# Kernel optimization log

Measured on AMD Instinct MI355X. Metric: run time of the kernel, lower is better.

Reference implementation:

```python
import jax, jax.numpy as jnp
import numpy as np
from jax import lax

N_HEADS = 16
EPS = 1e-6
CHUNK = 128  # chunk size for the causal kv cumsum scan


def causal_dot_product(q, k, v):
    """Equivalent to cumsum over outer-products: out[l] = q[l] . sum_{j<=l} k[j] v[j]^T.
    Chunked lax.scan avoids materializing the [B,H,L,D,M] tensor.
    q,k: [B,H,L,D], v: [B,H,L,M] -> [B,H,L,M]."""
    B, H, L, D = q.shape
    M = v.shape[-1]
    nc = L // CHUNK
    qc = q.reshape(B, H, nc, CHUNK, D).transpose(2, 0, 1, 3, 4)
    kc = k.reshape(B, H, nc, CHUNK, D).transpose(2, 0, 1, 3, 4)
    vc = v.reshape(B, H, nc, CHUNK, M).transpose(2, 0, 1, 3, 4)

    def step(kv_carry, inp):
        qb, kb, vb = inp  # [B,H,C,D], [B,H,C,D], [B,H,C,M]
        kv = jnp.einsum('bhcd,bhcm->bhcdm', kb, vb)
        kv_cum = jnp.cumsum(kv, axis=2) + kv_carry[:, :, None]
        out = jnp.einsum('bhcd,bhcdm->bhcm', qb, kv_cum)
        return kv_cum[:, :, -1], out

    init = jnp.zeros((B, H, D, M), q.dtype)
    _, outs = lax.scan(step, init, (qc, kc, vc))  # outs: [nc,B,H,C,M]
    return outs.transpose(1, 2, 0, 3, 4).reshape(B, H, L, M)


def flow_attention_causal(x, Wq, bq, Wk, bk, Wv, bv, Wo, bo):
    B, L, _ = x.shape
    d_model = Wq.shape[1]
    H = N_HEADS
    # projections -> [B,H,L,D]
    q = (x @ Wq + bq).reshape(B, L, H, -1).transpose(0, 2, 1, 3)
    k = (x @ Wk + bk).reshape(B, L, H, -1).transpose(0, 2, 1, 3)
    v = (x @ Wv + bv).reshape(B, L, H, -1).transpose(0, 2, 1, 3)
    # kernel_method = sigmoid
    q = jax.nn.sigmoid(q)
    k = jax.nn.sigmoid(k)

    sink_incoming = 1.0 / jnp.einsum('bhld,bhld->bhl', q + EPS, jnp.cumsum(k, axis=2) + EPS)
    source_outgoing = 1.0 / jnp.einsum('bhld,bhld->bhl', k + EPS, jnp.cumsum(q, axis=2) + EPS)
    normal = (jnp.arange(L, dtype=x.dtype) + 1.0)[None, None, :]  # [1,1,L]
    sink_incoming = sink_incoming * normal
    source_outgoing = source_outgoing * normal

    conserved_sink = jnp.einsum(
        'bhld,bhld->bhl', q + EPS,
        jnp.cumsum(k * source_outgoing[..., None], axis=2) + EPS) / normal
    conserved_source = jnp.einsum(
        'bhld,bhld->bhl', k + EPS,
        jnp.cumsum(q * sink_incoming[..., None], axis=2) + EPS) / normal

    sink_allocation = jax.nn.sigmoid(conserved_sink)
    cs = jnp.exp(conserved_source)
    source_competition = cs / jnp.cumsum(cs, axis=-1) * normal

    out = causal_dot_product(
        q * (sink_incoming / normal)[..., None],
        k,
        v * source_competition[..., None]) * sink_allocation[..., None]
    out = out.transpose(0, 2, 1, 3).reshape(B, L, d_model)
    return out @ Wo + bo  # dropout is identity at eval


def setup_inputs() -> dict:
    key = jax.random.key(0)
    ks = jax.random.split(key, 9)
    B, L, d_model = 4, 4096, 1024
    s = 0.02
    return {
        'x': jax.random.normal(ks[0], (B, L, d_model), dtype=jnp.float32),
        'Wq': jax.random.normal(ks[1], (d_model, d_model), dtype=jnp.float32) * s,
        'bq': jnp.zeros((d_model,), dtype=jnp.float32),
        'Wk': jax.random.normal(ks[2], (d_model, d_model), dtype=jnp.float32) * s,
        'bk': jnp.zeros((d_model,), dtype=jnp.float32),
        'Wv': jax.random.normal(ks[3], (d_model, d_model), dtype=jnp.float32) * s,
        'bv': jnp.zeros((d_model,), dtype=jnp.float32),
        'Wo': jax.random.normal(ks[4], (d_model, d_model), dtype=jnp.float32) * s,
        'bo': jnp.zeros((d_model,), dtype=jnp.float32),
    }


def reference(x, Wq, bq, Wk, bk, Wv, bv, Wo, bo):
    return flow_attention_causal(x, Wq, bq, Wk, bk, Wv, bv, Wo, bo)
```

## Files before the change

kernel.cpp:

```cpp
#include <hip/hip_runtime.h>
#include <stdint.h>

#define B_ 4
#define L_ 4096
#define DM 1024
#define H_ 16
#define D_ 64
#define BH (B_*H_)
#define N_ (B_*L_)
#define CS 128
#define NC (L_/CS)
#define SC 64
#define NSC (L_/SC)
#define EPSF 1e-6f

typedef unsigned short u16;
typedef unsigned int   u32;
typedef __attribute__((ext_vector_type(8))) short s16x8;
typedef __attribute__((ext_vector_type(4))) float f32x4;

__device__ __forceinline__ float bf2f(u16 u){
  union { u32 i; float f; } v; v.i = ((u32)u) << 16; return v.f;
}
__device__ __forceinline__ u16 f2bf(float f){
  union { float f; u32 i; } v; v.f = f;
  u32 i = v.i;
  return (u16)((i + 0x7fffu + ((i >> 16) & 1u)) >> 16);
}
__device__ __forceinline__ void gload16(const void* g, void* l){
  __builtin_amdgcn_global_load_lds(
      (const __attribute__((address_space(1))) u32*)g,
      (__attribute__((address_space(3))) u32*)l, 16, 0, 0);
}
__device__ __forceinline__ f32x4 mfma16(s16x8 a, s16x8 b, f32x4 c){
  return __builtin_amdgcn_mfma_f32_16x16x32_bf16(a, b, c, 0, 0, 0);
}
__device__ __forceinline__ float sigmoidf_(float x){ return 1.0f/(1.0f+__expf(-x)); }

__device__ __forceinline__ float prefix_sum64(const float* __restrict__ sums,
                                              int bh, int sc, int lane){
  float run = 0.f;
  for (int g = 0; g < NSC; g += 16){
    float tv[16];
    #pragma unroll
    for (int j = 0; j < 16; j++)
      tv[j] = sums[((size_t)bh*NSC + g + j)*64 + lane];
    #pragma unroll
    for (int j = 0; j < 16; j++)
      if (g + j < sc) run += tv[j];
  }
  return run;
}

__global__ __launch_bounds__(256) void prep_kernel(
    const float* __restrict__ x,
    const float* __restrict__ Wq, const float* __restrict__ Wk,
    const float* __restrict__ Wv, const float* __restrict__ Wo,
    u16* __restrict__ xb, u16* __restrict__ wqkvT, u16* __restrict__ woT){
  __shared__ float t[64][65];
  int bid = blockIdx.x;
  if (bid < 16384){
    int i = bid * 256 + threadIdx.x;
    float4 v = ((const float4*)x)[i];
    union { u16 s[4]; uint2 u; } o;
    o.s[0]=f2bf(v.x); o.s[1]=f2bf(v.y); o.s[2]=f2bf(v.z); o.s[3]=f2bf(v.w);
    ((uint2*)xb)[i] = o.u;
    return;
  }
  int w = bid - 16384;
  int z = w >> 8, w2 = w & 255;
  const float* W = (z==0) ? Wq : (z==1) ? Wk : (z==2) ? Wv : Wo;
  u16* WT = (z<3) ? (wqkvT + (size_t)z*DM*DM) : woT;
  int n0 = (w2 & 15) * 64, k0 = (w2 >> 4) * 64;
  int tx = threadIdx.x & 63, ty = threadIdx.x >> 6;
  #pragma unroll
  for (int s = 0; s < 64; s += 4)
    t[ty + s][tx] = W[(size_t)(k0 + ty + s) * DM + n0 + tx];
  __syncthreads();
  #pragma unroll
  for (int s = 0; s < 64; s += 4)
    WT[(size_t)(n0 + ty + s) * DM + k0 + tx] = f2bf(t[tx][ty + s]);
}

template<int QKV>
__global__ __launch_bounds__(512, 2) void gemm256_kernel(
    const u16* __restrict__ A, const u16* __restrict__ BT,
    const float* __restrict__ biasq, const float* __restrict__ biask, const float* __restrict__ biasv,
    u16* __restrict__ oq, u16* __restrict__ ok, u16* __restrict__ ov,
    float* __restrict__ outf,
    float* __restrict__ sumQ, float* __restrict__ sumK, int NBY)
{
  __shared__ __align__(16) u16 smem[65536];
  char* smb = (char*)smem;
  int tid = threadIdx.x;
  int wave = tid >> 6, lane = tid & 63;
  int wm = wave >> 2, wn = wave & 3;
  int nwg = gridDim.x;
  int q8 = nwg >> 3;
  int id = blockIdx.x;
  int id2 = (id & 7) * q8 + (id >> 3);
  int bx = id2 / NBY, by = id2 % NBY;
  int m0 = bx * 256, n0 = by * 256;
  int srcq = (tid & 7) ^ ((tid >> 3) & 7);
  const u16* aRow = A  + (size_t)(m0 + (tid >> 3)) * 1024 + srcq * 8;
  const u16* bRow = BT + (size_t)(n0 + (tid >> 3)) * 1024 + srcq * 8;

  f32x4 acc[8][4];
  #pragma unroll
  for (int i=0;i<8;i++)
    #pragma unroll
    for (int j=0;j<4;j++) acc[i][j] = (f32x4){0.f,0.f,0.f,0.f};

  int fr = lane & 15, q = lane >> 4;
  int aoff0 = fr*128 + (((q ^ (lane&3)) + 4*((lane>>2)&1)) << 4);
  int aoff1 = fr*128 + (((q ^ (lane&3)) + 4*(1 ^ ((lane>>2)&1))) << 4);

  #define STAGE(s, t) { \
    _Pragma("unroll") \
    for (int i_ = 0; i_ < 4; i_++){ \
      gload16(aRow + (size_t)(t)*64 + (size_t)i_*65536, smb + (s)*32768 + i_*8192 + tid*16); \
      gload16(bRow + (size_t)(t)*64 + (size_t)i_*65536, smb + 65536 + (s)*32768 + i_*8192 + tid*16); \
    } }

  #define COMPUTE(s) { \
    const char* Ab_ = smb + (s)*32768 + wm*16384; \
    const char* Bb_ = smb + 65536 + (s)*32768 + wn*8192; \
    _Pragma("unroll") \
    for (int kk_ = 0; kk_ < 2; kk_++){ \
      int off_ = kk_ ? aoff1 : aoff0; \
      s16x8 af_[8], bf_[4]; \
      _Pragma("unroll") \
      for (int mi_ = 0; mi_ < 8; mi_++) af_[mi_] = *(const s16x8*)(Ab_ + mi_*2048 + off_); \
      _Pragma("unroll") \
      for (int ni_ = 0; ni_ < 4; ni_++) bf_[ni_] = *(const s16x8*)(Bb_ + ni_*2048 + off_); \
      _Pragma("unroll") \
      for (int mi_ = 0; mi_ < 8; mi_++) \
        _Pragma("unroll") \
        for (int ni_ = 0; ni_ < 4; ni_++) \
          acc[mi_][ni_] = mfma16(af_[mi_], bf_[ni_], acc[mi_][ni_]); \
    } }

  STAGE(0, 0)
  STAGE(1, 1)
  for (int t = 0; t < 14; t++){
    asm volatile("s_waitcnt vmcnt(8)" ::: "memory");
    __builtin_amdgcn_s_barrier();
    asm volatile("" ::: "memory");
    COMPUTE(t & 1)
    asm volatile("s_waitcnt lgkmcnt(0)" ::: "memory");
    __builtin_amdgcn_s_barrier();
    asm volatile("" ::: "memory");
    STAGE(t & 1, t + 2)
  }
  asm volatile("s_waitcnt vmcnt(8)" ::: "memory");
  __builtin_amdgcn_s_barrier();
  asm volatile("" ::: "memory");
  COMPUTE(0)
  asm volatile("s_waitcnt vmcnt(0)" ::: "memory");
  __builtin_amdgcn_s_barrier();
  asm volatile("" ::: "memory");
  COMPUTE(1)

  int colblk = n0 + wn*64;
  int which  = QKV ? (colblk >> 10) : 0;
  int cl0    = QKV ? (colblk & 1023) : colblk;
  const float* bias = QKV ? (which==0 ? biasq : (which==1 ? biask : biasv)) : biasq;
  u16* outp = QKV ? (which==0 ? oq : (which==1 ? ok : ov)) : (u16*)0;
  float cs0[4] = {0.f,0.f,0.f,0.f}, cs1[4] = {0.f,0.f,0.f,0.f};
  #pragma unroll
  for (int mi = 0; mi < 8; mi++){
    int row = m0 + wm*128 + mi*16 + (lane>>4)*4;
    #pragma unroll
    for (int ni = 0; ni < 4; ni++){
      int cl = cl0 + ni*16 + fr;
      float bv = bias[cl];
      #pragma unroll
      for (int r = 0; r < 4; r++){
        float val = acc[mi][ni][r] + bv;
        if (QKV){
          if (which < 2) val = sigmoidf_(val);
          outp[(size_t)(row + r) * 1024 + cl] = f2bf(val);
          if (which < 2){ if (mi < 4) cs0[ni] += val; else cs1[ni] += val; }
        } else {
          outf[(size_t)(row + r) * 1024 + cl] = val;
        }
      }
    }
  }
  if (QKV && which < 2){
    float* sums = (which==0) ? sumQ : sumK;
    int bh = (m0 >> 12) * H_ + ((colblk & 1023) >> 6);
    int sc0 = ((m0 & 4095) >> 6) + wm*2;
    #pragma unroll
    for (int h2 = 0; h2 < 2; h2++){
      #pragma unroll
      for (int ni = 0; ni < 4; ni++){
        float s = h2 ? cs1[ni] : cs0[ni];
        s += __shfl_xor(s, 16);
        s += __shfl_xor(s, 32);
        if (lane < 16) sums[((size_t)bh*NSC + sc0 + h2)*64 + ni*16 + fr] = s;
      }
    }
  }
  #undef STAGE
  #undef COMPUTE
}

__global__ __launch_bounds__(128) void siso_fused_kernel(
    const u16* __restrict__ q, const u16* __restrict__ k,
    const float* __restrict__ sumQ, const float* __restrict__ sumK,
    float* __restrict__ si, float* __restrict__ so,
    float* __restrict__ sumQsi, float* __restrict__ sumKso)
{
  __shared__ u16 cq[64*64];
  __shared__ u16 ck[64*64];
  __shared__ float siv[64], sov[64];
  int bhc = blockIdx.x; int bh = bhc >> 6, sc = bhc & 63;
  int b = bh >> 4, h = bh & 15;
  int tid = threadIdx.x, w = tid >> 6, lane = tid & 63;
  size_t gbase = ((size_t)(b*L_ + sc*SC))*DM + h*D_;
  size_t lb = (size_t)bh*L_ + sc*SC;
  const u16* src = w ? k : q;
  u16* ldsT = w ? ck : cq;
  float run = prefix_sum64(w ? sumK : sumQ, bh, sc, lane);
  {
    int r8 = lane >> 3, c8 = (lane & 7) * 8;
    #pragma unroll
    for (int j = 0; j < 8; j++){
      int l = j*8 + r8;
      uint4 u = *(const uint4*)(src + gbase + (size_t)l*DM + c8);
      const u16* up = (const u16*)&u;
      #pragma unroll
      for (int e = 0; e < 8; e++)
        ldsT[l*64 + ((c8 + e) ^ (l & 31))] = up[e];
    }
  }
  __syncthreads();
  {
    for (int l = 0; l < SC; l++){
      int sw = lane ^ (l & 31);
      run += bf2f(ldsT[l*64 + sw]);
      ldsT[l*64 + sw] = f2bf(run);
    }
  }
  __syncthreads();
  uint4 rowreg[8];
  {
    int l = lane;
    const u16* row = src + gbase + (size_t)l*DM;
    #pragma unroll
    for (int j=0;j<8;j++) rowreg[j] = ((const uint4*)row)[j];
    const u16* rp = (const u16*)rowreg;
    const u16* other = w ? cq : ck;
    float acc = 0.f;
    #pragma unroll
    for (int d = 0; d < 64; d++){
      int sw = d ^ (l & 31);
      acc += (bf2f(rp[d])+EPSF) * (bf2f(other[l*64+sw])+EPSF);
    }
    float n = (float)(sc*SC + l + 1);
    float vv = n / acc;
    if (w == 0){ si[lb+l] = vv; siv[l] = vv; }
    else       { so[lb+l] = vv; sov[l] = vv; }
  }
  __syncthreads();
  {
    int l = lane;
    const u16* rp = (const u16*)rowreg;
    #pragma unroll
    for (int d = 0; d < 64; d++)
      ldsT[l*64 + (d ^ (l & 31))] = rp[d];
  }
  __syncthreads();
  {
    const float* sv = w ? sov : siv;
    float s = 0.f;
    for (int l = 0; l < SC; l++){
      int sw = lane ^ (l & 31);
      s += bf2f(ldsT[l*64 + sw]) * sv[l];
    }
    if (w == 0) sumQsi[bhc*64 + lane] = s;
    else        sumKso[bhc*64 + lane] = s;
  }
}

__global__ __launch_bounds__(128) void cons_fused_kernel(
    const u16* __restrict__ q, const u16* __restrict__ k,
    const float* __restrict__ si, const float* __restrict__ so,
    const float* __restrict__ sumQsi, const float* __restrict__ sumKso,
    float* __restrict__ csrc, float* __restrict__ sall, float* __restrict__ csSum)
{
  __shared__ u16 cq[64*64];
  __shared__ u16 ck[64*64];
  __shared__ float siv[64], sov[64];
  int bhc = blockIdx.x; int bh = bhc >> 6, sc = bhc & 63;
  int b = bh >> 4, h = bh & 15;
  int tid = threadIdx.x, w = tid >> 6, lane = tid & 63;
  size_t gbase = ((size_t)(b*L_ + sc*SC))*DM + h*D_;
  size_t lb = (size_t)bh*L_ + sc*SC;
  const u16* src = w ? k : q;
  u16* ldsT = w ? ck : cq;
  if (w == 0) siv[lane] = si[lb + lane];
  else        sov[lane] = so[lb + lane];
  float run = prefix_sum64(w ? sumKso : sumQsi, bh, sc, lane);
  {
    int r8 = lane >> 3, c8 = (lane & 7) * 8;
    #pragma unroll
    for (int j = 0; j < 8; j++){
      int l = j*8 + r8;
      uint4 u = *(const uint4*)(src + gbase + (size_t)l*DM + c8);
      const u16* up = (const u16*)&u;
      #pragma unroll
      for (int e = 0; e < 8; e++)
        ldsT[l*64 + ((c8 + e) ^ (l & 31))] = up[e];
    }
  }
  __syncthreads();
  {
    const float* sv = w ? sov : siv;
    for (int l = 0; l < SC; l++){
      int sw = lane ^ (l & 31);
      run += bf2f(ldsT[l*64 + sw]) * sv[l];
      ldsT[l*64 + sw] = f2bf(run);
    }
  }
  __syncthreads();
  {
    int l = lane;
    const u16* row = src + gbase + (size_t)l*DM;
    uint4 rr[8];
    #pragma unroll
    for (int j=0;j<8;j++) rr[j] = ((const uint4*)row)[j];
    const u16* rp = (const u16*)rr;
    const u16* other = w ? cq : ck;
    float acc = 0.f;
    #pragma unroll
    for (int d = 0; d < 64; d++){
      int sw = d ^ (l & 31);
      acc += (bf2f(rp[d])+EPSF) * (bf2f(other[l*64+sw])+EPSF);
    }
    float inv = 1.0f / (float)(sc*SC + l + 1);
    if (w == 0){
      sall[lb+l] = sigmoidf_(acc * inv);
    } else {
      float cs = acc * inv;
      csrc[lb+l] = cs;
      float e = __expf(cs);
      #pragma unroll
      for (int off = 32; off > 0; off >>= 1) e += __shfl_xor(e, off);
      if (lane == 0) csSum[bhc] = e;
    }
  }
}

__global__ __launch_bounds__(256) void vk_chunk_kernel(
    const u16* __restrict__ k, const u16* __restrict__ v,
    const float* __restrict__ csrc, const float* __restrict__ csSum,
    float* __restrict__ scomp, float* __restrict__ vkc){
  __shared__ __align__(16) u16 vt[64*128];
  __shared__ __align__(16) u16 kt[64*128];
  __shared__ float scmpv[128];
  int bhc = blockIdx.x; int bh = bhc >> 5, c = bhc & 31;
  int b = bh >> 4, h = bh & 15;
  int tid = threadIdx.x, wave = tid >> 6, lane = tid & 63;
  size_t gbase = ((size_t)(b * L_ + c * CS)) * DM + h * D_;
  if (wave < 2){
    int sc = c*2 + wave;
    float v2 = (lane < sc) ? csSum[bh*NSC + lane] : 0.f;
    #pragma unroll
    for (int o = 32; o > 0; o >>= 1) v2 += __shfl_xor(v2, o);
    float off = v2;
    size_t idx = (size_t)bh * L_ + sc * SC + lane;
    float cs = __expf(csrc[idx]);
    float run = cs;
    #pragma unroll
    for (int o = 1; o < 64; o <<= 1){
      float t = __shfl_up(run, o);
      if (lane >= o) run += t;
    }
    float sm = cs / (off + run) * (float)(sc*SC + lane + 1);
    scomp[idx] = sm;
    scmpv[wave*64 + lane] = sm;
  }
  __syncthreads();
  {
    int r = tid >> 1;
    int cc = (tid & 1) * 32;
    float vscale = scmpv[r];
    #pragma unroll
    for (int j = 0; j < 4; j++){
      uint4 ku = *(const uint4*)(k + gbase + (size_t)r * DM + cc + j*8);
      uint4 vu = *(const uint4*)(v + gbase + (size_t)r * DM + cc + j*8);
      const u16* kp = (const u16*)&ku; const u16* vp = (const u16*)&vu;
      #pragma unroll
      for (int e = 0; e < 8; e++){
        int m = cc + j*8 + e;
        int idx = m*128 + ((((r >> 3) ^ (m & 7)) << 3) | (r & 7));
        vt[idx] = f2bf(bf2f(vp[e]) * vscale);
        kt[idx] = kp[e];
      }
    }
  }
  __syncthreads();
  int fr = lane & 15, q = lane >> 4;
  int mt = wave;
  f32x4 acc[4];
  #pragma unroll
  for (int i = 0; i < 4; i++) acc[i] = (f32x4){0.f,0.f,0.f,0.f};
  #pragma unroll
  for (int ks = 0; ks < 4; ks++){
    int lc = ks*4 + q;
    int off = ((lc ^ (fr & 7)) << 3);
    s16x8 av = *(const s16x8*)&vt[(mt*16 + fr)*128 + off];
    #pragma unroll
    for (int nt = 0; nt < 4; nt++){
      s16x8 bk = *(const s16x8*)&kt[(nt*16 + fr)*128 + off];
      acc[nt] = mfma16(av, bk, acc[nt]);
    }
  }
  float* outp = vkc + (size_t)bhc * (D_*D_);
  #pragma unroll
  for (int nt = 0; nt < 4; nt++)
    #pragma unroll
    for (int r = 0; r < 4; r++)
      outp[(mt*16 + q*4 + r)*64 + nt*16 + fr] = acc[nt][r];
}

__global__ __launch_bounds__(256) void vk_scan_kernel(const float* __restrict__ vkc, u16* __restrict__ vkb){
  int idx = blockIdx.x * 256 + threadIdx.x;
  int bh = idx >> 12;
  int e  = idx & 4095;
  size_t base = ((size_t)bh * NC) * 4096 + e;
  float run = 0.f;
  for (int g = 0; g < NC; g += 16){
    float tv[16];
    #pragma unroll
    for (int j = 0; j < 16; j++) tv[j] = vkc[base + (size_t)(g + j) * 4096];
    #pragma unroll
    for (int j = 0; j < 16; j++){
      vkb[base + (size_t)(g + j) * 4096] = f2bf(run);
      run += tv[j];
    }
  }
}

__global__ __launch_bounds__(256) void attn_kernel(
    const u16* __restrict__ q, const u16* __restrict__ k, const u16* __restrict__ v,
    const float* __restrict__ si, const float* __restrict__ scomp, const float* __restrict__ salloc,
    const u16* __restrict__ vkb, u16* __restrict__ attnout)
{
  __shared__ __align__(16) u16 qs[128*64];
  __shared__ __align__(16) u16 ks2[128*64];
  __shared__ __align__(16) u16 vts[64*128];
  __shared__ __align__(16) u16 vks[64*64];
  __shared__ __align__(16) u16 ss[128*64];
  int bhc = blockIdx.x; int bh = bhc >> 5, c = bhc & 31;
  int b = bh >> 4, h = bh & 15;
  int tid = threadIdx.x, wave = tid >> 6, lane = tid & 63;
  size_t gbase = ((size_t)(b * L_ + c * CS)) * DM + h * D_;
  size_t sbase = (size_t)bh * L_ + c * CS;
  {
    int r = tid >> 1;
    int cc = (tid & 1) * 32;
    int l = c * CS + r;
    float qscale = si[sbase + r] / (float)(l + 1);
    float vscale = scomp[sbase + r];
    #pragma unroll
    for (int j = 0; j < 4; j++){
      int d0 = cc + j*8;
      uint4 qu = *(const uint4*)(q + gbase + (size_t)r * DM + d0);
      uint4 kuv = *(const uint4*)(k + gbase + (size_t)r * DM + d0);
      uint4 vu = *(const uint4*)(v + gbase + (size_t)r * DM + d0);
      const u16* qp = (const u16*)&qu; const u16* vp = (const u16*)&vu;
      u16 tmp[8];
      #pragma unroll
      for (int e = 0; e < 8; e++) tmp[e] = f2bf(bf2f(qp[e]) * qscale);
      int csw = ((d0 >> 3) ^ (r & 7)) << 3;
      *(uint4*)&qs[r*64 + csw]  = *(uint4*)tmp;
      *(uint4*)&ks2[r*64 + csw] = kuv;
      #pragma unroll
      for (int e = 0; e < 8; e++){
        int m = d0 + e;
        int jsw = (((r >> 3) ^ (m & 7)) << 3) | (r & 7);
        vts[m*128 + jsw] = f2bf(bf2f(vp[e]) * vscale);
      }
    }
    const u16* vkp = vkb + (size_t)bhc * (D_*D_) + tid * 16;
    int m = tid >> 2, dq = (tid & 3) * 2;
    int o0 = ((dq     ^ (m & 7)) << 3);
    int o1 = (((dq+1) ^ (m & 7)) << 3);
    *(uint4*)&vks[m*64 + o0] = *(const uint4*)(vkp);
    *(uint4*)&vks[m*64 + o1] = *(const uint4*)(vkp + 8);
  }
  __syncthreads();
  int t0 = wave, t1 = 7 - wave;
  int fr = lane & 15, qh = lane >> 4;
  int f7 = fr & 7;
  f32x4 acc[2][4];
  #pragma unroll
  for (int i=0;i<2;i++)
    #pragma unroll
    for (int j=0;j<4;j++) acc[i][j] = (f32x4){0.f,0.f,0.f,0.f};
  s16x8 aq[2][2];
  #pragma unroll
  for (int ti = 0; ti < 2; ti++){
    int t = ti ? t1 : t0;
    #pragma unroll
    for (int kk = 0; kk < 2; kk++){
      int oc = (((kk*4 + qh) ^ f7) << 3);
      aq[ti][kk] = *(const s16x8*)&qs[(t*16 + fr)*64 + oc];
    }
  }
  #pragma unroll
  for (int mt = 0; mt < 4; mt++){
    #pragma unroll
    for (int kk = 0; kk < 2; kk++){
      int oc = (((kk*4 + qh) ^ f7) << 3);
      s16x8 bv = *(const s16x8*)&vks[(mt*16 + fr)*64 + oc];
      acc[0][mt] = mfma16(aq[0][kk], bv, acc[0][mt]);
      acc[1][mt] = mfma16(aq[1][kk], bv, acc[1][mt]);
    }
  }
  for (int jt2 = 0; jt2 < 2; jt2++){
    __syncthreads();
    #pragma unroll
    for (int ti = 0; ti < 2; ti++){
      int t = ti ? t1 : t0;
      #pragma unroll
      for (int u = 0; u < 4; u++){
        int jj = jt2*4 + u;
        f32x4 sacc = (f32x4){0.f,0.f,0.f,0.f};
        if (jj <= t){
          #pragma unroll
          for (int kk = 0; kk < 2; kk++){
            int oc = (((kk*4 + qh) ^ f7) << 3);
            s16x8 bkf = *(const s16x8*)&ks2[(jj*16 + fr)*64 + oc];
            sacc = mfma16(aq[ti][kk], bkf, sacc);
          }
        }
        int lrow = t*16 + qh*4;
        int jcol = jj*16 + fr;
        int cst = u*2 + (fr >> 3);
        #pragma unroll
        for (int r = 0; r < 4; r++){
          float sv = (jcol <= lrow + r) ? sacc[r] : 0.f;
          int row = lrow + r;
          ss[row*64 + (((cst ^ (row & 7)) << 3) | f7)] = f2bf(sv);
        }
      }
    }
    __syncthreads();
    #pragma unroll
    for (int ti = 0; ti < 2; ti++){
      int t = ti ? t1 : t0;
      #pragma unroll
      for (int ks = 0; ks < 2; ks++){
        if (jt2*64 + ks*32 <= t*16 + 15){
          int ocs = (((ks*4 + qh) ^ f7) << 3);
          s16x8 as = *(const s16x8*)&ss[(t*16 + fr)*64 + ocs];
          #pragma unroll
          for (int mt = 0; mt < 4; mt++){
            int lc = jt2*8 + ks*4 + qh;
            int ocv = ((lc ^ f7) << 3);
            s16x8 bvv = *(const s16x8*)&vts[(mt*16 + fr)*128 + ocv];
            acc[ti][mt] = mfma16(as, bvv, acc[ti][mt]);
          }
        }
      }
    }
  }
  #pragma unroll
  for (int ti = 0; ti < 2; ti++){
    int t = ti ? t1 : t0;
    int lrow = t*16 + qh*4;
    #pragma unroll
    for (int r = 0; r < 4; r++){
      float sa = salloc[sbase + lrow + r];
      size_t orow = ((size_t)(b * L_ + c * CS + lrow + r)) * DM + h * D_;
      #pragma unroll
      for (int mt = 0; mt < 4; mt++){
        attnout[orow + mt*16 + fr] = f2bf(acc[ti][mt][r] * sa);
      }
    }
  }
}

extern "C" void kernel_launch(void* const* d_in, const int* in_sizes, int n_in,
                              void* d_out, int out_size, void* d_ws, size_t ws_size,
                              hipStream_t stream){
  (void)in_sizes; (void)n_in; (void)out_size; (void)ws_size;
  const float* x  = (const float*)d_in[0];
  const float* Wq = (const float*)d_in[1];
  const float* bq = (const float*)d_in[2];
  const float* Wk = (const float*)d_in[3];
  const float* bk = (const float*)d_in[4];
  const float* Wv = (const float*)d_in[5];
  const float* bv = (const float*)d_in[6];
  const float* Wo = (const float*)d_in[7];
  const float* bo = (const float*)d_in[8];

  char* p = (char*)d_ws;
  auto carve = [&](size_t bytes) -> void* {
    void* r = (void*)p; p += (bytes + 255) & ~(size_t)255; return r;
  };
  u16* xb    = (u16*)carve((size_t)N_*DM*2);
  u16* wqkvT = (u16*)carve((size_t)3*DM*DM*2);
  u16* woT   = (u16*)carve((size_t)DM*DM*2);
  u16* qb  = (u16*)carve((size_t)N_*DM*2);
  u16* kb  = (u16*)carve((size_t)N_*DM*2);
  u16* vb  = (u16*)carve((size_t)N_*DM*2);
  u16* ao  = (u16*)carve((size_t)N_*DM*2);
  float* si   = (float*)carve((size_t)BH*L_*4);
  float* so   = (float*)carve((size_t)BH*L_*4);
  float* csrc = (float*)carve((size_t)BH*L_*4);
  float* sall = (float*)carve((size_t)BH*L_*4);
  float* scmp = (float*)carve((size_t)BH*L_*4);
  float* sumQ   = (float*)carve((size_t)BH*NSC*D_*4);
  float* sumK   = (float*)carve((size_t)BH*NSC*D_*4);
  float* sumQsi = (float*)carve((size_t)BH*NSC*D_*4);
  float* sumKso = (float*)carve((size_t)BH*NSC*D_*4);
  float* csSum  = (float*)carve((size_t)BH*NSC*4);
  float* vkc    = (float*)carve((size_t)BH*NC*(size_t)(D_*D_)*4);
  u16*   vkb    = (u16*)carve((size_t)BH*NC*(size_t)(D_*D_)*2);

  prep_kernel<<<16384 + 4*256, 256, 0, stream>>>(x, Wq, Wk, Wv, Wo, xb, wqkvT, woT);
  gemm256_kernel<1><<<dim3((N_/256)*(3*DM/256)), 512, 0, stream>>>(
      xb, wqkvT, bq, bk, bv, qb, kb, vb, nullptr, sumQ, sumK, 3*DM/256);
  siso_fused_kernel<<<BH*NSC, 128, 0, stream>>>(qb, kb, sumQ, sumK, si, so, sumQsi, sumKso);
  cons_fused_kernel<<<BH*NSC, 128, 0, stream>>>(qb, kb, si, so, sumQsi, sumKso, csrc, sall, csSum);
  vk_chunk_kernel<<<BH*NC, 256, 0, stream>>>(kb, vb, csrc, csSum, scmp, vkc);
  vk_scan_kernel<<<(BH*D_*D_)/256, 256, 0, stream>>>(vkc, vkb);
  attn_kernel<<<BH*NC, 256, 0, stream>>>(qb, kb, vb, si, scmp, sall, vkb, ao);
  gemm256_kernel<0><<<dim3((N_/256)*(DM/256)), 512, 0, stream>>>(
      ao, woT, bo, bo, bo, nullptr, nullptr, nullptr, (float*)d_out, nullptr, nullptr, DM/256);
}
```

Before: 313.3 us.

## Store per-chunk KV states in bf16 and double-buffer attention score tile

The per-chunk V^T K partial states are now written and read as bf16 instead of fp32, halving the traffic between the chunk and scan kernels. In the attention kernel the score tile is double-buffered, with the first half written into the already-consumed Q shared buffer, which removes one barrier between the QK and PV phases. The bf16 partials add rounding error to the running sum. Reusing the Q buffer relies on the new barrier placed after the Q fragments are loaded into registers.

```diff
diff --git a/kernel.cpp b/kernel.cpp
--- a/kernel.cpp
+++ b/kernel.cpp
@@ -356,7 +356,7 @@
 __global__ __launch_bounds__(256) void vk_chunk_kernel(
     const u16* __restrict__ k, const u16* __restrict__ v,
     const float* __restrict__ csrc, const float* __restrict__ csSum,
-    float* __restrict__ scomp, float* __restrict__ vkc){
+    float* __restrict__ scomp, u16* __restrict__ vkc16){
   __shared__ __align__(16) u16 vt[64*128];
   __shared__ __align__(16) u16 kt[64*128];
   __shared__ float scmpv[128];
@@ -418,28 +418,28 @@
       acc[nt] = mfma16(av, bk, acc[nt]);
     }
   }
-  float* outp = vkc + (size_t)bhc * (D_*D_);
+  u16* outp = vkc16 + (size_t)bhc * (D_*D_);
   #pragma unroll
   for (int nt = 0; nt < 4; nt++)
     #pragma unroll
     for (int r = 0; r < 4; r++)
-      outp[(mt*16 + q*4 + r)*64 + nt*16 + fr] = acc[nt][r];
-}
-
-__global__ __launch_bounds__(256) void vk_scan_kernel(const float* __restrict__ vkc, u16* __restrict__ vkb){
+      outp[(mt*16 + q*4 + r)*64 + nt*16 + fr] = f2bf(acc[nt][r]);
+}
+
+__global__ __launch_bounds__(256) void vk_scan_kernel(const u16* __restrict__ vkc16, u16* __restrict__ vkb){
   int idx = blockIdx.x * 256 + threadIdx.x;
   int bh = idx >> 12;
   int e  = idx & 4095;
   size_t base = ((size_t)bh * NC) * 4096 + e;
   float run = 0.f;
   for (int g = 0; g < NC; g += 16){
-    float tv[16];
-    #pragma unroll
-    for (int j = 0; j < 16; j++) tv[j] = vkc[base + (size_t)(g + j) * 4096];
+    u16 tv[16];
+    #pragma unroll
+    for (int j = 0; j < 16; j++) tv[j] = vkc16[base + (size_t)(g + j) * 4096];
     #pragma unroll
     for (int j = 0; j < 16; j++){
       vkb[base + (size_t)(g + j) * 4096] = f2bf(run);
-      run += tv[j];
+      run += bf2f(tv[j]);
     }
   }
 }
@@ -511,6 +511,7 @@
       aq[ti][kk] = *(const s16x8*)&qs[(t*16 + fr)*64 + oc];
     }
   }
+  __syncthreads();
   #pragma unroll
   for (int mt = 0; mt < 4; mt++){
     #pragma unroll
@@ -521,54 +522,60 @@
       acc[1][mt] = mfma16(aq[1][kk], bv, acc[1][mt]);
     }
   }
-  for (int jt2 = 0; jt2 < 2; jt2++){
-    __syncthreads();
-    #pragma unroll
-    for (int ti = 0; ti < 2; ti++){
-      int t = ti ? t1 : t0;
-      #pragma unroll
-      for (int u = 0; u < 4; u++){
-        int jj = jt2*4 + u;
-        f32x4 sacc = (f32x4){0.f,0.f,0.f,0.f};
-        if (jj <= t){
-          #pragma unroll
-          for (int kk = 0; kk < 2; kk++){
-            int oc = (((kk*4 + qh) ^ f7) << 3);
-            s16x8 bkf = *(const s16x8*)&ks2[(jj*16 + fr)*64 + oc];
-            sacc = mfma16(aq[ti][kk], bkf, sacc);
-          }
-        }
-        int lrow = t*16 + qh*4;
-        int jcol = jj*16 + fr;
-        int cst = u*2 + (fr >> 3);
-        #pragma unroll
-        for (int r = 0; r < 4; r++){
-          float sv = (jcol <= lrow + r) ? sacc[r] : 0.f;
-          int row = lrow + r;
-          ss[row*64 + (((cst ^ (row & 7)) << 3) | f7)] = f2bf(sv);
-        }
-      }
-    }
-    __syncthreads();
-    #pragma unroll
-    for (int ti = 0; ti < 2; ti++){
-      int t = ti ? t1 : t0;
-      #pragma unroll
-      for (int ks = 0; ks < 2; ks++){
-        if (jt2*64 + ks*32 <= t*16 + 15){
-          int ocs = (((ks*4 + qh) ^ f7) << 3);
-          s16x8 as = *(const s16x8*)&ss[(t*16 + fr)*64 + ocs];
-          #pragma unroll
-          for (int mt = 0; mt < 4; mt++){
-            int lc = jt2*8 + ks*4 + qh;
-            int ocv = ((lc ^ f7) << 3);
-            s16x8 bvv = *(const s16x8*)&vts[(mt*16 + fr)*128 + ocv];
-            acc[ti][mt] = mfma16(as, bvv, acc[ti][mt]);
-          }
-        }
-      }
-    }
-  }
+  #define QK_HALF(jt2, dst) \
+    _Pragma("unroll") \
+    for (int ti = 0; ti < 2; ti++){ \
+      int t = ti ? t1 : t0; \
+      _Pragma("unroll") \
+      for (int u = 0; u < 4; u++){ \
+        int jj = (jt2)*4 + u; \
+        f32x4 sacc = (f32x4){0.f,0.f,0.f,0.f}; \
+        if (jj <= t){ \
+          _Pragma("unroll") \
+          for (int kk = 0; kk < 2; kk++){ \
+            int oc = (((kk*4 + qh) ^ f7) << 3); \
+            s16x8 bkf = *(const s16x8*)&ks2[(jj*16 + fr)*64 + oc]; \
+            sacc = mfma16(aq[ti][kk], bkf, sacc); \
+          } \
+        } \
+        int lrow = t*16 + qh*4; \
+        int jcol = jj*16 + fr; \
+        int cst = u*2 + (fr >> 3); \
+        _Pragma("unroll") \
+        for (int r = 0; r < 4; r++){ \
+          float sv = (jcol <= lrow + r) ? sacc[r] : 0.f; \
+          int row = lrow + r; \
+          dst[row*64 + (((cst ^ (row & 7)) << 3) | f7)] = f2bf(sv); \
+        } \
+      } \
+    }
+  #define PV_HALF(jt2, srcb) \
+    _Pragma("unroll") \
+    for (int ti = 0; ti < 2; ti++){ \
+      int t = ti ? t1 : t0; \
+      _Pragma("unroll") \
+      for (int ks = 0; ks < 2; ks++){ \
+        if ((jt2)*64 + ks*32 <= t*16 + 15){ \
+          int ocs = (((ks*4 + qh) ^ f7) << 3); \
+          s16x8 as = *(const s16x8*)&srcb[(t*16 + fr)*64 + ocs]; \
+          _Pragma("unroll") \
+          for (int mt = 0; mt < 4; mt++){ \
+            int lc = (jt2)*8 + ks*4 + qh; \
+            int ocv = ((lc ^ f7) << 3); \
+            s16x8 bvv = *(const s16x8*)&vts[(mt*16 + fr)*128 + ocv]; \
+            acc[ti][mt] = mfma16(as, bvv, acc[ti][mt]); \
+          } \
+        } \
+      } \
+    }
+  QK_HALF(0, qs)
+  __syncthreads();
+  QK_HALF(1, ss)
+  PV_HALF(0, qs)
+  __syncthreads();
+  PV_HALF(1, ss)
+  #undef QK_HALF
+  #undef PV_HALF
   #pragma unroll
   for (int ti = 0; ti < 2; ti++){
     int t = ti ? t1 : t0;
@@ -620,7 +627,7 @@
   float* sumQsi = (float*)carve((size_t)BH*NSC*D_*4);
   float* sumKso = (float*)carve((size_t)BH*NSC*D_*4);
   float* csSum  = (float*)carve((size_t)BH*NSC*4);
-  float* vkc    = (float*)carve((size_t)BH*NC*(size_t)(D_*D_)*4);
+  u16*   vkc16  = (u16*)carve((size_t)BH*NC*(size_t)(D_*D_)*2);
   u16*   vkb    = (u16*)carve((size_t)BH*NC*(size_t)(D_*D_)*2);
 
   prep_kernel<<<16384 + 4*256, 256, 0, stream>>>(x, Wq, Wk, Wv, Wo, xb, wqkvT, woT);
@@ -628,8 +635,8 @@
       xb, wqkvT, bq, bk, bv, qb, kb, vb, nullptr, sumQ, sumK, 3*DM/256);
   siso_fused_kernel<<<BH*NSC, 128, 0, stream>>>(qb, kb, sumQ, sumK, si, so, sumQsi, sumKso);
   cons_fused_kernel<<<BH*NSC, 128, 0, stream>>>(qb, kb, si, so, sumQsi, sumKso, csrc, sall, csSum);
-  vk_chunk_kernel<<<BH*NC, 256, 0, stream>>>(kb, vb, csrc, csSum, scmp, vkc);
-  vk_scan_kernel<<<(BH*D_*D_)/256, 256, 0, stream>>>(vkc, vkb);
+  vk_chunk_kernel<<<BH*NC, 256, 0, stream>>>(kb, vb, csrc, csSum, scmp, vkc16);
+  vk_scan_kernel<<<(BH*D_*D_)/256, 256, 0, stream>>>(vkc16, vkb);
   attn_kernel<<<BH*NC, 256, 0, stream>>>(qb, kb, vb, si, scmp, sall, vkb, ao);
   gemm256_kernel<0><<<dim3((N_/256)*(DM/256)), 512, 0, stream>>>(
       ao, woT, bo, bo, bo, nullptr, nullptr, nullptr, (float*)d_out, nullptr, nullptr, DM/256);
```

Measured after the change: 307.8 us, median of 2. No clear change (-1.7%).
